# Performance work log

Measured on AMD Instinct MI355X. Metric: run time of the kernel, lower is better.

The kernel has to match this reference:

```python
import jax, jax.numpy as jnp
import numpy as np

# distilled LLaVA-style decoder: nf4-quantized linears + LoRA(q/k/v/o) + gumbel-softmax -> embedding einsum
B, S, D, H, L = 1, 2048, 2048, 16, 2
DH = D // H
DFF, V, R, BLK = 8192, 32000, 8, 64
LORA_SCALE = 16.0 / R  # alpha / r
TAU = 1.0
SQRT_DH = float(np.sqrt(DH))

# bitsandbytes NF4 codebook (16 values)
NF4 = jnp.array([-1.0, -0.6961928009986877, -0.5250730514526367, -0.39491748809814453,
                 -0.28444138169288635, -0.18477343022823334, -0.09105003625154495, 0.0,
                 0.07958029955625534, 0.16093020141124725, 0.24611230194568634,
                 0.33791524171829224, 0.44070982933044434, 0.5626170039176941,
                 0.7229568362236023, 1.0], dtype=jnp.float32)


def dequant(idx, scale):
    # idx [..., out, in] int in [0,16); scale [..., out, in//BLK] per-block absmax
    return NF4[idx] * jnp.repeat(scale, BLK, axis=-1)


def rmsnorm(x, w):
    return x * jax.lax.rsqrt(jnp.mean(x * x, axis=-1, keepdims=True) + 1e-6) * w


def setup_inputs():
    key = jax.random.key(0)
    k = jax.random.split(key, 12)
    return {
        "input_ids": jax.random.randint(k[0], (B, S), 0, V, dtype=jnp.int32),
        "u": jax.random.uniform(k[1], (B, S, V), dtype=jnp.float32),
        "emb": jax.random.normal(k[2], (V, D), dtype=jnp.float32) * 0.02,
        "attn_scale": jax.random.uniform(k[3], (L, 4, D, D // BLK), minval=0.005, maxval=0.02, dtype=jnp.float32),
        "ffn_gu_scale": jax.random.uniform(k[4], (L, 2, DFF, D // BLK), minval=0.005, maxval=0.02, dtype=jnp.float32),
        "ffn_d_scale": jax.random.uniform(k[5], (L, D, DFF // BLK), minval=0.005, maxval=0.02, dtype=jnp.float32),
        "lora_A": jax.random.normal(k[6], (L, 4, R, D), dtype=jnp.float32) * 0.01,
        "lora_B": jax.random.normal(k[7], (L, 4, D, R), dtype=jnp.float32) * 0.01,
        "norm_w": jnp.ones((L, 2, D), dtype=jnp.float32),
        "final_norm_w": jnp.ones((D,), dtype=jnp.float32),
        "attn_idx": jax.random.randint(k[8], (L, 4, D, D), 0, 16, dtype=jnp.int32),
        "ffn_gu_idx": jax.random.randint(k[9], (L, 2, DFF, D), 0, 16, dtype=jnp.int32),
        "ffn_d_idx": jax.random.randint(k[10], (L, D, DFF), 0, 16, dtype=jnp.int32),
    }


def reference(input_ids, u, emb, attn_scale, ffn_gu_scale, ffn_d_scale,
              lora_A, lora_B, norm_w, final_norm_w, attn_idx, ffn_gu_idx, ffn_d_idx):
    h = emb[input_ids]  # [B, S, D]
    causal = jnp.tril(jnp.ones((S, S), dtype=bool))
    for l in range(L):
        x = rmsnorm(h, norm_w[l, 0])
        w = dequant(attn_idx[l], attn_scale[l])  # [4, D, D] dequantized q/k/v/o weights

        def proj(i, t):
            # nf4 linear + LoRA adapter (y = t W^T + (t A^T) B^T * alpha/r)
            return t @ w[i].T + ((t @ lora_A[l, i].T) @ lora_B[l, i].T) * LORA_SCALE

        q = proj(0, x).reshape(B, S, H, DH)
        k_ = proj(1, x).reshape(B, S, H, DH)
        v = proj(2, x).reshape(B, S, H, DH)
        scores = jnp.einsum('bqhd,bkhd->bhqk', q, k_) / SQRT_DH
        scores = jnp.where(causal, scores, -1e30)
        p = jax.nn.softmax(scores, axis=-1)
        o = jnp.einsum('bhqk,bkhd->bqhd', p, v).reshape(B, S, D)
        h = h + proj(3, o)

        x = rmsnorm(h, norm_w[l, 1])
        wgu = dequant(ffn_gu_idx[l], ffn_gu_scale[l])  # [2, DFF, D] gate/up
        wd = dequant(ffn_d_idx[l], ffn_d_scale[l])     # [D, DFF] down
        h = h + (jax.nn.silu(x @ wgu[0].T) * (x @ wgu[1].T)) @ wd.T

    h = rmsnorm(h, final_norm_w)
    logits = h @ emb.T  # [B, S, V]
    # gumbel_softmax(tau, hard=False): softmax((logits + G)/tau), G = -log(-log(U))
    gnoise = -jnp.log(-jnp.log(u + 1e-10) + 1e-10)
    g = jax.nn.softmax((logits + gnoise) / TAU, axis=-1)
    soft_embeddings = jnp.einsum('bsv,vd->bsd', g, emb)
    return soft_embeddings, logits
```

## Files before the change

### kernel.cpp

```cpp
#include <hip/hip_runtime.h>
#include <hip/hip_bf16.h>

typedef unsigned short u16;
typedef unsigned int u32;
typedef __bf16 bf16t;
typedef bf16t bf16x8 __attribute__((ext_vector_type(8)));
typedef float f32x4 __attribute__((ext_vector_type(4)));

constexpr int S_   = 2048;
constexpr int D_   = 2048;
constexpr int H_   = 16;
constexpr int DH_  = 128;
constexpr int L_   = 2;
constexpr int DFF_ = 8192;
constexpr int V_   = 32000;
constexpr int R_   = 8;

#define MFMA16(a, b, c) __builtin_amdgcn_mfma_f32_16x16x32_bf16(a, b, c, 0, 0, 0)

__constant__ float c_nf4[16] = {
  -1.0f, -0.6961928009986877f, -0.5250730514526367f, -0.39491748809814453f,
  -0.28444138169288635f, -0.18477343022823334f, -0.09105003625154495f, 0.0f,
  0.07958029955625534f, 0.16093020141124725f, 0.24611230194568634f,
  0.33791524171829224f, 0.44070982933044434f, 0.5626170039176941f,
  0.7229568362236023f, 1.0f };

__device__ __forceinline__ u16 f2bf(float f) {
  union { float f; u32 u; } v; v.f = f;
  u32 r = v.u + 0x7fffu + ((v.u >> 16) & 1u);
  return (u16)(r >> 16);
}
__device__ __forceinline__ float bf2f(u16 h) {
  union { u32 u; float f; } v; v.u = ((u32)h) << 16; return v.f;
}

__global__ __launch_bounds__(256) void k_gather(const int* __restrict__ ids,
                                                const float* __restrict__ emb,
                                                float* __restrict__ h) {
  int t = blockIdx.x * 256 + threadIdx.x;
  int s = t >> 11;
  int d = t & 2047;
  h[t] = emb[(size_t)ids[s] * D_ + d];
}

__global__ __launch_bounds__(256) void k_rmsnorm(const float* __restrict__ in,
                                                 const float* __restrict__ w,
                                                 u16* __restrict__ out) {
  int s = blockIdx.x;
  const float* x = in + (size_t)s * D_;
  float ss = 0.f;
  for (int d = threadIdx.x; d < D_; d += 256) { float v = x[d]; ss += v * v; }
#pragma unroll
  for (int m = 1; m < 64; m <<= 1) ss += __shfl_xor(ss, m, 64);
  __shared__ float sh[4];
  if ((threadIdx.x & 63) == 0) sh[threadIdx.x >> 6] = ss;
  __syncthreads();
  ss = sh[0] + sh[1] + sh[2] + sh[3];
  float sc = rsqrtf(ss * (1.0f / D_) + 1e-6f);
  u16* o = out + (size_t)s * D_;
  for (int d = threadIdx.x; d < D_; d += 256) o[d] = f2bf(x[d] * sc * w[d]);
}

__global__ __launch_bounds__(256) void k_dequant(const int* __restrict__ idx,
                                                 const float* __restrict__ scale,
                                                 u16* __restrict__ out, int kshift) {
  size_t t = (size_t)blockIdx.x * 256 + threadIdx.x;
  size_t e = t * 8;
  int k = (int)(e & ((1u << kshift) - 1));
  size_t n = e >> kshift;
  float s = scale[(n << (kshift - 6)) + (k >> 6)];
  int4 i0 = *(const int4*)(idx + e);
  int4 i1 = *(const int4*)(idx + e + 4);
  uint4 o;
  o.x = (u32)f2bf(c_nf4[i0.x] * s) | ((u32)f2bf(c_nf4[i0.y] * s) << 16);
  o.y = (u32)f2bf(c_nf4[i0.z] * s) | ((u32)f2bf(c_nf4[i0.w] * s) << 16);
  o.z = (u32)f2bf(c_nf4[i1.x] * s) | ((u32)f2bf(c_nf4[i1.y] * s) << 16);
  o.w = (u32)f2bf(c_nf4[i1.z] * s) | ((u32)f2bf(c_nf4[i1.w] * s) << 16);
  *(uint4*)(out + e) = o;
}

__global__ __launch_bounds__(256) void k_f2b(const float* __restrict__ src,
                                             u16* __restrict__ dst) {
  size_t e = ((size_t)blockIdx.x * 256 + threadIdx.x) * 8;
  float4 f0 = *(const float4*)(src + e);
  float4 f1 = *(const float4*)(src + e + 4);
  uint4 o;
  o.x = (u32)f2bf(f0.x) | ((u32)f2bf(f0.y) << 16);
  o.y = (u32)f2bf(f0.z) | ((u32)f2bf(f0.w) << 16);
  o.z = (u32)f2bf(f1.x) | ((u32)f2bf(f1.y) << 16);
  o.w = (u32)f2bf(f1.z) | ((u32)f2bf(f1.w) << 16);
  *(uint4*)(dst + e) = o;
}

__global__ __launch_bounds__(256) void k_transpose(const float* __restrict__ src,
                                                   u16* __restrict__ dst) {
  __shared__ u16 tile[64][65];
  int v0 = blockIdx.x * 64, d0 = blockIdx.y * 64;
  int tid = threadIdx.x;
  int rr = tid >> 4, cc = (tid & 15) * 4;
#pragma unroll
  for (int j = 0; j < 4; ++j) {
    int r = j * 16 + rr;
    float4 f = *(const float4*)(src + (size_t)(v0 + r) * D_ + d0 + cc);
    tile[r][cc + 0] = f2bf(f.x); tile[r][cc + 1] = f2bf(f.y);
    tile[r][cc + 2] = f2bf(f.z); tile[r][cc + 3] = f2bf(f.w);
  }
  __syncthreads();
#pragma unroll
  for (int j = 0; j < 4; ++j) {
    int r = j * 16 + rr;
    ushort4 w;
    w.x = tile[cc + 0][r]; w.y = tile[cc + 1][r];
    w.z = tile[cc + 2][r]; w.w = tile[cc + 3][r];
    *(ushort4*)(dst + (size_t)(d0 + r) * V_ + v0 + cc) = w;
  }
}

enum { OUT_F32 = 0, OUT_F32_ACC = 1, OUT_BF16 = 2 };

template<int OUTMODE>
__global__ __launch_bounds__(512, 2) void k_gemm256(const u16* __restrict__ A, int lda,
                                                    const u16* __restrict__ B, int ldb,
                                                    void* __restrict__ Cv, int ldc,
                                                    int Kc, size_t zstride) {
  __shared__ u16 As[2][256][64];
  __shared__ u16 Bs[2][256][64];
  const int tid = threadIdx.x;
  const int lane = tid & 63, w = tid >> 6;
  const int wr = w >> 2, wc = w & 3;
  const int g = (lane >> 4), l15 = lane & 15, sl7 = lane & 7;

  const int gx = gridDim.x, gy = gridDim.y;
  const int cpx = (gx * gy) >> 3;
  int d = blockIdx.y * gx + blockIdx.x;
  int swz = (d & 7) * cpx + (d >> 3);
  const int m0 = (swz % gy) * 256;
  const int n0 = (swz / gy) * 256;

  A += (size_t)blockIdx.z * Kc;
  B += (size_t)blockIdx.z * Kc;
  float* Cf = (float*)Cv + (size_t)blockIdx.z * zstride;

  const int NT = Kc >> 6;
  const int srow = w * 8 + (lane >> 3);
  const int sch  = (lane & 7) ^ (lane >> 3);

  auto stageA = [&](int half, int tile) {
    const u16* src = A + (size_t)(m0 + half * 128 + srow) * lda + tile * 64 + sch * 8;
    u16* dst = &As[tile & 1][half * 128 + w * 8][0];
#pragma unroll
    for (int rnd = 0; rnd < 2; ++rnd)
      __builtin_amdgcn_global_load_lds(
          (const __attribute__((address_space(1))) void*)(src + (size_t)rnd * 64 * lda),
          (__attribute__((address_space(3))) void*)(dst + rnd * 64 * 64), 16, 0, 0);
  };
  auto stageB = [&](int half, int tile) {
    const u16* src = B + (size_t)(n0 + half * 128 + srow) * ldb + tile * 64 + sch * 8;
    u16* dst = &Bs[tile & 1][half * 128 + w * 8][0];
#pragma unroll
    for (int rnd = 0; rnd < 2; ++rnd)
      __builtin_amdgcn_global_load_lds(
          (const __attribute__((address_space(1))) void*)(src + (size_t)rnd * 64 * ldb),
          (__attribute__((address_space(3))) void*)(dst + rnd * 64 * 64), 16, 0, 0);
  };

  f32x4 acc[8][4] = {};
  bf16x8 areg[4][2], breg[2][2][2];

  stageB(0, 0); stageB(1, 0); stageA(0, 0); stageA(1, 0);
  if (NT > 1) {
    stageB(0, 1); stageB(1, 1); stageA(0, 1); stageA(1, 1);
    asm volatile("s_waitcnt vmcnt(8)" ::: "memory");
  } else {
    asm volatile("s_waitcnt vmcnt(0)" ::: "memory");
  }
  __builtin_amdgcn_s_barrier();

#define LOADA(QR)                                                                   \
  _Pragma("unroll") for (int m = 0; m < 4; ++m)                                     \
    _Pragma("unroll") for (int kh = 0; kh < 2; ++kh) {                              \
      int hr = wr * 128 + (QR) * 64 + m * 16 + l15;                                 \
      areg[m][kh] = *(const bf16x8*)(abase + hr * 64 + ((((kh << 2) | g) ^ sl7) << 3)); \
    }
#define LOADB(QC)                                                                   \
  _Pragma("unroll") for (int n = 0; n < 2; ++n)                                     \
    _Pragma("unroll") for (int kh = 0; kh < 2; ++kh) {                              \
      int br = wc * 64 + (QC) * 32 + n * 16 + l15;                                  \
      breg[QC][n][kh] = *(const bf16x8*)(bbase + br * 64 + ((((kh << 2) | g) ^ sl7) << 3)); \
    }
#define QPHASE(QR, QC)                                                              \
  __builtin_amdgcn_s_setprio(1);                                                    \
  _Pragma("unroll") for (int m = 0; m < 4; ++m)                                     \
    _Pragma("unroll") for (int n = 0; n < 2; ++n)                                   \
      _Pragma("unroll") for (int kh = 0; kh < 2; ++kh)                              \
        acc[(QR) * 4 + m][(QC) * 2 + n] = __builtin_amdgcn_mfma_f32_16x16x32_bf16(  \
            areg[m][kh], breg[QC][n][kh], acc[(QR) * 4 + m][(QC) * 2 + n], 0, 0, 0); \
  __builtin_amdgcn_s_setprio(0);

  for (int t = 0; t < NT; ++t) {
    const u16* abase = &As[t & 1][0][0];
    const u16* bbase = &Bs[t & 1][0][0];
    LOADA(0); LOADB(0);
    __builtin_amdgcn_s_barrier();
    asm volatile("s_waitcnt lgkmcnt(0)" ::: "memory");
    QPHASE(0, 0);
    __builtin_amdgcn_s_barrier();
    LOADB(1);
    __builtin_amdgcn_s_barrier();
    asm volatile("s_waitcnt lgkmcnt(0)" ::: "memory");
    QPHASE(0, 1);
    __builtin_amdgcn_s_barrier();
    LOADA(1);
    if (t + 2 < NT) { stageB(0, t + 2); stageB(1, t + 2); }
    __builtin_amdgcn_s_barrier();
    asm volatile("s_waitcnt lgkmcnt(0)" ::: "memory");
    QPHASE(1, 1);
    __builtin_amdgcn_s_barrier();
    if (t + 2 < NT) { stageA(0, t + 2); stageA(1, t + 2); }
    QPHASE(1, 0);
    if (t + 1 < NT) {
      if (t + 2 < NT) asm volatile("s_waitcnt vmcnt(8)" ::: "memory");
      else            asm volatile("s_waitcnt vmcnt(0)" ::: "memory");
    }
    __builtin_amdgcn_s_barrier();
  }
#undef LOADA
#undef LOADB
#undef QPHASE

  const int er = g * 4;
#pragma unroll
  for (int i = 0; i < 8; ++i)
#pragma unroll
    for (int j = 0; j < 4; ++j)
#pragma unroll
      for (int r = 0; r < 4; ++r) {
        int row = m0 + wr * 128 + i * 16 + er + r;
        int col = n0 + wc * 64 + j * 16 + l15;
        if (OUTMODE == OUT_BF16) {
          ((u16*)Cv)[(size_t)row * ldc + col] = f2bf(acc[i][j][r]);
        } else if (OUTMODE == OUT_F32_ACC) {
          Cf[(size_t)row * ldc + col] += acc[i][j][r];
        } else {
          Cf[(size_t)row * ldc + col] = acc[i][j][r];
        }
      }
}

__global__ __launch_bounds__(256) void k_red(const float* __restrict__ P,
                                             float* __restrict__ dst, int accmode) {
  size_t i = ((size_t)blockIdx.x * 256 + threadIdx.x) * 4;
  const size_t n = (size_t)4 * 1024 * 1024;
  float4 a = *(const float4*)(P + i);
  float4 b = *(const float4*)(P + n + i);
  float4 c = *(const float4*)(P + 2 * n + i);
  float4 d = *(const float4*)(P + 3 * n + i);
  float4 r;
  r.x = (a.x + b.x) + (c.x + d.x);
  r.y = (a.y + b.y) + (c.y + d.y);
  r.z = (a.z + b.z) + (c.z + d.z);
  r.w = (a.w + b.w) + (c.w + d.w);
  if (accmode) {
    float4 o = *(const float4*)(dst + i);
    r.x += o.x; r.y += o.y; r.z += o.z; r.w += o.w;
  }
  *(float4*)(dst + i) = r;
}

__global__ __launch_bounds__(256) void k_lora_down(const u16* __restrict__ X,
                                                   const float* __restrict__ A,
                                                   float* __restrict__ T, int nproj) {
  int s = blockIdx.x;
  int lane = threadIdx.x & 63, wv = threadIdx.x >> 6;
  const u16* x = X + (size_t)s * D_;
  for (int p = wv; p < nproj * R_; p += 4) {
    const float* a = A + (size_t)p * D_;
    float sum = 0.f;
    for (int d = lane; d < D_; d += 64) sum += bf2f(x[d]) * a[d];
#pragma unroll
    for (int m = 1; m < 64; m <<= 1) sum += __shfl_xor(sum, m, 64);
    if (lane == 0) T[(size_t)s * (nproj * R_) + p] = sum;
  }
}

__global__ __launch_bounds__(256) void k_lora_up(float* __restrict__ Y, int ystride,
                                                 const float* __restrict__ T,
                                                 const float* __restrict__ Bm, int nproj) {
  int t = blockIdx.x * 256 + threadIdx.x;
  int d = t & (D_ - 1);
  int si = t >> 11;
  int i = si % nproj;
  int s = si / nproj;
  const float* tp = T + ((size_t)s * nproj + i) * R_;
  const float* bp = Bm + ((size_t)i * D_ + d) * R_;
  float acc = 0.f;
#pragma unroll
  for (int r = 0; r < R_; r++) acc += tp[r] * bp[r];
  Y[(size_t)s * ystride + (size_t)i * D_ + d] += 2.0f * acc;
}

__global__ __launch_bounds__(256) void k_lora_up_qkv(u16* __restrict__ qkvb,
                                                     const float* __restrict__ T,
                                                     const float* __restrict__ Bm) {
  size_t t = ((size_t)blockIdx.x * 256 + threadIdx.x) * 8;
  int c = (int)(t % 6144);
  int s = (int)(t / 6144);
  int i = c >> 11, dd = c & 2047;
  const float* tp = T + ((size_t)s * 3 + i) * R_;
  float tr[8];
#pragma unroll
  for (int r = 0; r < R_; ++r) tr[r] = tp[r];
  uint4 q = *(const uint4*)(qkvb + t);
  u16 qs[8] = {(u16)(q.x & 0xffff), (u16)(q.x >> 16), (u16)(q.y & 0xffff), (u16)(q.y >> 16),
               (u16)(q.z & 0xffff), (u16)(q.z >> 16), (u16)(q.w & 0xffff), (u16)(q.w >> 16)};
  u16 os[8];
#pragma unroll
  for (int j = 0; j < 8; ++j) {
    const float* bp = Bm + ((size_t)i * D_ + dd + j) * R_;
    float a = 0.f;
#pragma unroll
    for (int r = 0; r < R_; ++r) a += tr[r] * bp[r];
    os[j] = f2bf(bf2f(qs[j]) + 2.0f * a);
  }
  uint4 o;
  o.x = (u32)os[0] | ((u32)os[1] << 16);
  o.y = (u32)os[2] | ((u32)os[3] << 16);
  o.z = (u32)os[4] | ((u32)os[5] << 16);
  o.w = (u32)os[6] | ((u32)os[7] << 16);
  *(uint4*)(qkvb + t) = o;
}

__global__ __launch_bounds__(256) void k_vtrans(const u16* __restrict__ qkvb,
                                                u16* __restrict__ Vt) {
  __shared__ u16 t[64][136];
  int s0 = blockIdx.x * 64, hh = blockIdx.y;
  int tid = threadIdx.x;
#pragma unroll
  for (int it = 0; it < 4; ++it) {
    int e = it * 2048 + tid * 8;
    int sr = e >> 7, sc = e & 127;
    *(uint4*)&t[sr][sc] =
        *(const uint4*)(qkvb + (size_t)(s0 + sr) * 6144 + 4096 + hh * 128 + sc);
  }
  __syncthreads();
#pragma unroll
  for (int it = 0; it < 4; ++it) {
    int q = it * 256 + tid;
    int dh = q >> 3, sc = (q & 7) * 8;
    u16 e0 = t[sc + 0][dh], e1 = t[sc + 1][dh], e2 = t[sc + 2][dh], e3 = t[sc + 3][dh];
    u16 e4 = t[sc + 4][dh], e5 = t[sc + 5][dh], e6 = t[sc + 6][dh], e7 = t[sc + 7][dh];
    uint4 o;
    o.x = (u32)e0 | ((u32)e1 << 16);
    o.y = (u32)e2 | ((u32)e3 << 16);
    o.z = (u32)e4 | ((u32)e5 << 16);
    o.w = (u32)e6 | ((u32)e7 << 16);
    *(uint4*)(Vt + ((size_t)hh * DH_ + dh) * S_ + s0 + sc) = o;
  }
}

__global__ __launch_bounds__(256) void k_attn2(const u16* __restrict__ qkvb,
                                               const u16* __restrict__ Vt,
                                               u16* __restrict__ out) {
  __shared__ u16 Ks[2][64 * 128];
  __shared__ u16 VTs[2][128 * 64];
  __shared__ u16 PT[4][64 * 16];
  const int tid = threadIdx.x;
  const int lane = tid & 63, w = tid >> 6;
  const int g = lane >> 4, l4 = lane & 15;
  const int p = blockIdx.x;
  const int hh = blockIdx.y;
  const int ld = 6144;
  const float rs = 0.08838834764831845f;
  const int qa0 = p * 64, qb0 = (31 - p) * 64;
  const int ntb = 32 - p;
  char* pt_w = (char*)&PT[w][0];

  const int qga = qa0 + w * 16 + l4;
  const int qgb = qb0 + w * 16 + l4;

  bf16x8 qfa[4], qfb[4];
#pragma unroll
  for (int kh = 0; kh < 4; ++kh) {
    qfa[kh] = *(const bf16x8*)(qkvb + (size_t)qga * ld + hh * DH_ + kh * 32 + g * 8);
    qfb[kh] = *(const bf16x8*)(qkvb + (size_t)qgb * ld + hh * DH_ + kh * 32 + g * 8);
  }

  float ma = -3.0e38f, la = 0.f, mb = -3.0e38f, lb = 0.f;
  f32x4 acc_a[8] = {}, acc_b[8] = {};
  bf16x8 pba[2], pbb[2];

  auto stage = [&](int buf, int kt) {
    const int kv0 = kt * 64;
#pragma unroll
    for (int i = 0; i < 4; ++i) {
      int rl = (w * 4 + i) * 4 + (lane >> 4);
      int cs = (lane & 15) ^ ((rl & 7) ^ (((rl >> 3) & 3) << 1));
      __builtin_amdgcn_global_load_lds(
          (const __attribute__((address_space(1))) void*)(
              qkvb + (size_t)(kv0 + rl) * ld + 2048 + hh * DH_ + cs * 8),
          (__attribute__((address_space(3))) void*)(&Ks[buf][(w * 4 + i) * 512]), 16, 0, 0);
    }
#pragma unroll
    for (int i = 0; i < 4; ++i) {
      int dh = (w * 4 + i) * 8 + (lane >> 3);
      int cs = (lane & 7) ^ (dh & 7);
      __builtin_amdgcn_global_load_lds(
          (const __attribute__((address_space(1))) void*)(
              Vt + ((size_t)hh * DH_ + dh) * S_ + kv0 + cs * 8),
          (__attribute__((address_space(3))) void*)(&VTs[buf][(w * 4 + i) * 512]), 16, 0, 0);
    }
  };

  auto softpb = [&](f32x4* sv, float& m, float& l, f32x4* acc, int qg, bool diag,
                    int kv0, bf16x8* pb) {
    float pv[16];
    float tmax = -3.0e38f;
#pragma unroll
    for (int kb = 0; kb < 4; ++kb)
#pragma unroll
      for (int r = 0; r < 4; ++r) {
        float s = sv[kb][r] * rs;
        if (diag) {
          int kglob = kv0 + kb * 16 + g * 4 + r;
          if (kglob > qg) s = -1.0e30f;
        }
        pv[kb * 4 + r] = s;
        tmax = fmaxf(tmax, s);
      }
    tmax = fmaxf(tmax, __shfl_xor(tmax, 16, 64));
    tmax = fmaxf(tmax, __shfl_xor(tmax, 32, 64));
    float mn = fmaxf(m, tmax);
    float corr = __expf(m - mn);
    m = mn;
    float ps = 0.f;
#pragma unroll
    for (int i = 0; i < 16; ++i) { pv[i] = __expf(pv[i] - mn); ps += pv[i]; }
    ps += __shfl_xor(ps, 16, 64);
    ps += __shfl_xor(ps, 32, 64);
    l = l * corr + ps;
#pragma unroll
    for (int f = 0; f < 8; ++f) {
      acc[f][0] *= corr; acc[f][1] *= corr; acc[f][2] *= corr; acc[f][3] *= corr;
    }
#pragma unroll
    for (int kb = 0; kb < 4; ++kb)
#pragma unroll
      for (int r = 0; r < 4; ++r) {
        int key = kb * 16 + g * 4 + r;
        int byte = (key * 32 + l4 * 2) ^ (((key >> 3) & 3) << 5);
        *(u16*)(pt_w + byte) = f2bf(pv[kb * 4 + r]);
      }
#pragma unroll
    for (int ks = 0; ks < 2; ++ks) {
      union { bf16x8 v; u16 s[8]; } ub;
#pragma unroll
      for (int j = 0; j < 8; ++j) {
        int key = ks * 32 + g * 8 + j;
        int byte = (key * 32 + l4 * 2) ^ (((key >> 3) & 3) << 5);
        ub.s[j] = *(const u16*)(pt_w + byte);
      }
      pb[ks] = ub.v;
    }
  };

  stage(0, 0);
  asm volatile("s_waitcnt vmcnt(0)" ::: "memory");
  __syncthreads();

  for (int kt = 0; kt < ntb; ++kt) {
    const int kv0 = kt * 64;
    const int buf = kt & 1;
    if (kt + 1 < ntb) stage(buf ^ 1, kt + 1);

    const char* kb_base = (const char*)&Ks[buf][0];
    const char* vb_base = (const char*)&VTs[buf][0];
    const bool doa = (kt <= p);

    f32x4 sa[4] = {}, sb[4] = {};
#pragma unroll
    for (int kb = 0; kb < 4; ++kb) {
#pragma unroll
      for (int kh = 0; kh < 4; ++kh) {
        int key = kb * 16 + l4;
        int ch = (kh * 4 + g) ^ ((key & 7) ^ (((key >> 3) & 3) << 1));
        bf16x8 af = *(const bf16x8*)(kb_base + key * 256 + ch * 16);
        if (doa) sa[kb] = MFMA16(af, qfa[kh], sa[kb]);
        sb[kb] = MFMA16(af, qfb[kh], sb[kb]);
      }
    }

    if (doa) softpb(sa, ma, la, acc_a, qga, kt == p, kv0, pba);
    softpb(sb, mb, lb, acc_b, qgb, kt == ntb - 1, kv0, pbb);

#pragma unroll
    for (int f = 0; f < 8; ++f) {
#pragma unroll
      for (int ks = 0; ks < 2; ++ks) {
        int dh = f * 16 + l4;
        int ch = (ks * 4 + g) ^ (dh & 7);
        bf16x8 va = *(const bf16x8*)(vb_base + dh * 128 + ch * 16);
        if (doa) acc_a[f] = MFMA16(va, pba[ks], acc_a[f]);
        acc_b[f] = MFMA16(va, pbb[ks], acc_b[f]);
      }
    }

    if (kt + 1 < ntb) {
      asm volatile("s_waitcnt vmcnt(0)" ::: "memory");
      __syncthreads();
    }
  }

  float inva = 1.f / la, invb = 1.f / lb;
  u16* opa = out + (size_t)qga * D_ + hh * DH_;
  u16* opb = out + (size_t)qgb * D_ + hh * DH_;
#pragma unroll
  for (int f = 0; f < 8; ++f)
#pragma unroll
    for (int r = 0; r < 4; ++r) {
      opa[f * 16 + g * 4 + r] = f2bf(acc_a[f][r] * inva);
      opb[f * 16 + g * 4 + r] = f2bf(acc_b[f][r] * invb);
    }
}

__global__ __launch_bounds__(256) void k_silumul(u16* __restrict__ gu) {
  size_t i = ((size_t)blockIdx.x * 256 + threadIdx.x) * 4;
  int s = (int)(i >> 13);
  int f = (int)(i & 8191);
  u16* gp = gu + (size_t)s * (2 * DFF_) + f;
  ushort4 gt = *(ushort4*)gp;
  ushort4 up = *(ushort4*)(gp + DFF_);
  float g0 = bf2f(gt.x), g1 = bf2f(gt.y), g2 = bf2f(gt.z), g3 = bf2f(gt.w);
  float u0 = bf2f(up.x), u1 = bf2f(up.y), u2 = bf2f(up.z), u3 = bf2f(up.w);
  ushort4 o;
  o.x = f2bf(g0 / (1.f + __expf(-g0)) * u0);
  o.y = f2bf(g1 / (1.f + __expf(-g1)) * u1);
  o.z = f2bf(g2 / (1.f + __expf(-g2)) * u2);
  o.w = f2bf(g3 / (1.f + __expf(-g3)) * u3);
  *(ushort4*)gp = o;
}

__global__ __launch_bounds__(256) void k_gumbel(const float* __restrict__ logits,
                                                const float* __restrict__ u,
                                                u16* __restrict__ g) {
  __shared__ float z[V_];
  __shared__ float sred[4];
  int s = blockIdx.x;
  const float* lp = logits + (size_t)s * V_;
  const float* up = u + (size_t)s * V_;
  float m = -3.0e38f;
  for (int v4 = threadIdx.x; v4 < V_ / 4; v4 += 256) {
    float4 lv = *(const float4*)(lp + v4 * 4);
    float4 uv = *(const float4*)(up + v4 * 4);
    float z0 = lv.x - __logf(-__logf(uv.x + 1e-10f) + 1e-10f);
    float z1 = lv.y - __logf(-__logf(uv.y + 1e-10f) + 1e-10f);
    float z2 = lv.z - __logf(-__logf(uv.z + 1e-10f) + 1e-10f);
    float z3 = lv.w - __logf(-__logf(uv.w + 1e-10f) + 1e-10f);
    *(float4*)(z + v4 * 4) = make_float4(z0, z1, z2, z3);
    m = fmaxf(fmaxf(fmaxf(m, z0), fmaxf(z1, z2)), z3);
  }
#pragma unroll
  for (int msk = 1; msk < 64; msk <<= 1) m = fmaxf(m, __shfl_xor(m, msk, 64));
  if ((threadIdx.x & 63) == 0) sred[threadIdx.x >> 6] = m;
  __syncthreads();
  float M = fmaxf(fmaxf(sred[0], sred[1]), fmaxf(sred[2], sred[3]));
  float l = 0.f;
  for (int v4 = threadIdx.x; v4 < V_ / 4; v4 += 256) {
    float4 zv = *(float4*)(z + v4 * 4);
    zv.x = __expf(zv.x - M); zv.y = __expf(zv.y - M);
    zv.z = __expf(zv.z - M); zv.w = __expf(zv.w - M);
    *(float4*)(z + v4 * 4) = zv;
    l += (zv.x + zv.y) + (zv.z + zv.w);
  }
#pragma unroll
  for (int msk = 1; msk < 64; msk <<= 1) l += __shfl_xor(l, msk, 64);
  __syncthreads();
  if ((threadIdx.x & 63) == 0) sred[threadIdx.x >> 6] = l;
  __syncthreads();
  float inv = 1.f / (sred[0] + sred[1] + sred[2] + sred[3]);
  u16* gp = g + (size_t)s * V_;
  for (int v4 = threadIdx.x; v4 < V_ / 4; v4 += 256) {
    float4 zv = *(float4*)(z + v4 * 4);
    ushort4 o;
    o.x = f2bf(zv.x * inv); o.y = f2bf(zv.y * inv);
    o.z = f2bf(zv.z * inv); o.w = f2bf(zv.w * inv);
    *(ushort4*)(gp + v4 * 4) = o;
  }
}

extern "C" void kernel_launch(void* const* d_in, const int* in_sizes, int n_in,
                              void* d_out, int out_size, void* d_ws, size_t ws_size,
                              hipStream_t stream) {
  const int*   ids        = (const int*)d_in[0];
  const float* u          = (const float*)d_in[1];
  const float* emb        = (const float*)d_in[2];
  const float* attn_scale = (const float*)d_in[3];
  const float* gu_scale   = (const float*)d_in[4];
  const float* dn_scale   = (const float*)d_in[5];
  const float* lora_A     = (const float*)d_in[6];
  const float* lora_B     = (const float*)d_in[7];
  const float* norm_w     = (const float*)d_in[8];
  const float* fnorm_w    = (const float*)d_in[9];
  const int*   attn_idx   = (const int*)d_in[10];
  const int*   gu_idx     = (const int*)d_in[11];
  const int*   dn_idx     = (const int*)d_in[12];

  float* out_se = (float*)d_out;
  float* out_lg = (float*)d_out + (size_t)S_ * D_;

  char* W = (char*)d_ws;
  float* h    = (float*)(W);
  u16*   xb   = (u16*)(W + ((size_t)16 << 20));
  u16*   qkvb = (u16*)(W + ((size_t)72 << 20));
  u16*   Vtb  = (u16*)(W + ((size_t)96 << 20));
  u16*   ob   = (u16*)(W + ((size_t)104 << 20));
  u16*   gub  = (u16*)(W + ((size_t)112 << 20));
  u16*   wdq  = (u16*)(W + ((size_t)176 << 20));
  float* Tl   = (float*)(W + ((size_t)240 << 20));
  u16*   embb = (u16*)(W);
  u16*   gsm  = (u16*)(W + ((size_t)125 << 20));
  u16*   embT = (u16*)(W);
  u16*   xbh  = (u16*)d_out;
  float* Pk   = (float*)(W + ((size_t)250 << 20));
  const bool big = ws_size >= ((size_t)314 << 20);
  const size_t ZS = (size_t)4 * 1024 * 1024;

  dim3 b256(256), b512(512);

  k_gather<<<dim3(S_ * D_ / 256), b256, 0, stream>>>(ids, emb, h);

  for (int l = 0; l < L_; ++l) {
    const int*   aidx = attn_idx + (size_t)l * 4 * D_ * D_;
    const float* ascl = attn_scale + (size_t)l * 4 * D_ * (D_ / 64);
    const float* lA   = lora_A + (size_t)l * 4 * R_ * D_;
    const float* lB   = lora_B + (size_t)l * 4 * D_ * R_;

    k_rmsnorm<<<dim3(S_), b256, 0, stream>>>(h, norm_w + (size_t)l * 2 * D_, xb);
    k_dequant<<<dim3(4 * D_ * D_ / 8 / 256), b256, 0, stream>>>(aidx, ascl, wdq, 11);
    k_gemm256<OUT_BF16><<<dim3(3 * D_ / 256, 8), b512, 0, stream>>>(
        xb, D_, wdq, D_, qkvb, 3 * D_, D_, 0);
    k_lora_down<<<dim3(S_), b256, 0, stream>>>(xb, lA, Tl, 3);
    k_lora_up_qkv<<<dim3(S_ * 3 * D_ / 8 / 256), b256, 0, stream>>>(qkvb, Tl, lB);
    k_vtrans<<<dim3(S_ / 64, H_), b256, 0, stream>>>(qkvb, Vtb);
    k_attn2<<<dim3(16, H_), b256, 0, stream>>>(qkvb, Vtb, ob);
    k_gemm256<OUT_F32_ACC><<<dim3(D_ / 256, 8), b512, 0, stream>>>(
        ob, D_, wdq + (size_t)3 * D_ * D_, D_, h, D_, D_, 0);
    k_lora_down<<<dim3(S_), b256, 0, stream>>>(ob, lA + (size_t)3 * R_ * D_, Tl, 1);
    k_lora_up<<<dim3(S_ * D_ / 256), b256, 0, stream>>>(h, D_, Tl, lB + (size_t)3 * D_ * R_, 1);

    k_rmsnorm<<<dim3(S_), b256, 0, stream>>>(h, norm_w + (size_t)l * 2 * D_ + D_, xb);
    k_dequant<<<dim3(2 * DFF_ * D_ / 8 / 256), b256, 0, stream>>>(
        gu_idx + (size_t)l * 2 * DFF_ * D_, gu_scale + (size_t)l * 2 * DFF_ * (D_ / 64), wdq, 11);
    k_gemm256<OUT_BF16><<<dim3(2 * DFF_ / 256, 8), b512, 0, stream>>>(
        xb, D_, wdq, D_, gub, 2 * DFF_, D_, 0);
    k_silumul<<<dim3(S_ * DFF_ / 4 / 256), b256, 0, stream>>>(gub);
    k_dequant<<<dim3(D_ * DFF_ / 8 / 256), b256, 0, stream>>>(
        dn_idx + (size_t)l * D_ * DFF_, dn_scale + (size_t)l * D_ * (DFF_ / 64), wdq, 13);
    if (big) {
      k_gemm256<OUT_F32><<<dim3(D_ / 256, 8, 4), b512, 0, stream>>>(
          gub, 2 * DFF_, wdq, DFF_, Pk, D_, DFF_ / 4, ZS);
      k_red<<<dim3(4096), b256, 0, stream>>>(Pk, h, 1);
    } else {
      k_gemm256<OUT_F32_ACC><<<dim3(D_ / 256, 8), b512, 0, stream>>>(
          gub, 2 * DFF_, wdq, DFF_, h, D_, DFF_, 0);
    }
  }

  k_rmsnorm<<<dim3(S_), b256, 0, stream>>>(h, fnorm_w, xbh);
  k_f2b<<<dim3(V_ * D_ / 8 / 256), b256, 0, stream>>>(emb, embb);
  k_gemm256<OUT_F32><<<dim3(V_ / 256, 8), b512, 0, stream>>>(
      xbh, D_, embb, D_, out_lg, V_, D_, 0);
  k_gumbel<<<dim3(S_), b256, 0, stream>>>(out_lg, u, gsm);
  k_transpose<<<dim3(V_ / 64, D_ / 64), b256, 0, stream>>>(emb, embT);
  if (big) {
    k_gemm256<OUT_F32><<<dim3(D_ / 256, 8, 4), b512, 0, stream>>>(
        gsm, V_, embT, V_, Pk, D_, V_ / 4, ZS);
    k_red<<<dim3(4096), b256, 0, stream>>>(Pk, out_se, 0);
  } else {
    k_gemm256<OUT_F32><<<dim3(D_ / 256, 8), b512, 0, stream>>>(
        gsm, V_, embT, V_, out_se, D_, V_, 0);
  }
}
```

Measured before the change: 2.443 ms.

## Fuse embedding prep, split-K o-proj, and spread GEMM staging across phases

Merges the fp32->bf16 embedding conversion and the transpose into one kernel that writes both layouts from a single read of emb. To make room, the gsm and embT workspace buffers swap places. The GEMM now issues its global->LDS staging loads across all four compute phases instead of two, with vmcnt thresholds adjusted to match, and it changes the warp-to-subtile mapping so each quadrant is spread across warps. The attention output projection uses split-K with a reduction when the workspace is large, giving 64 blocks more parallelism at the cost of an extra reduction pass and partial-sum traffic.

```diff
diff --git a/kernel.cpp b/kernel.cpp
--- a/kernel.cpp
+++ b/kernel.cpp
@@ -79,21 +79,9 @@
   *(uint4*)(out + e) = o;
 }
 
-__global__ __launch_bounds__(256) void k_f2b(const float* __restrict__ src,
-                                             u16* __restrict__ dst) {
-  size_t e = ((size_t)blockIdx.x * 256 + threadIdx.x) * 8;
-  float4 f0 = *(const float4*)(src + e);
-  float4 f1 = *(const float4*)(src + e + 4);
-  uint4 o;
-  o.x = (u32)f2bf(f0.x) | ((u32)f2bf(f0.y) << 16);
-  o.y = (u32)f2bf(f0.z) | ((u32)f2bf(f0.w) << 16);
-  o.z = (u32)f2bf(f1.x) | ((u32)f2bf(f1.y) << 16);
-  o.w = (u32)f2bf(f1.z) | ((u32)f2bf(f1.w) << 16);
-  *(uint4*)(dst + e) = o;
-}
-
-__global__ __launch_bounds__(256) void k_transpose(const float* __restrict__ src,
-                                                   u16* __restrict__ dst) {
+__global__ __launch_bounds__(256) void k_embprep(const float* __restrict__ src,
+                                                 u16* __restrict__ embb,
+                                                 u16* __restrict__ embT) {
   __shared__ u16 tile[64][65];
   int v0 = blockIdx.x * 64, d0 = blockIdx.y * 64;
   int tid = threadIdx.x;
@@ -102,8 +90,11 @@
   for (int j = 0; j < 4; ++j) {
     int r = j * 16 + rr;
     float4 f = *(const float4*)(src + (size_t)(v0 + r) * D_ + d0 + cc);
-    tile[r][cc + 0] = f2bf(f.x); tile[r][cc + 1] = f2bf(f.y);
-    tile[r][cc + 2] = f2bf(f.z); tile[r][cc + 3] = f2bf(f.w);
+    u16 b0 = f2bf(f.x), b1 = f2bf(f.y), b2 = f2bf(f.z), b3 = f2bf(f.w);
+    tile[r][cc + 0] = b0; tile[r][cc + 1] = b1;
+    tile[r][cc + 2] = b2; tile[r][cc + 3] = b3;
+    ushort4 wv; wv.x = b0; wv.y = b1; wv.z = b2; wv.w = b3;
+    *(ushort4*)(embb + (size_t)(v0 + r) * D_ + d0 + cc) = wv;
   }
   __syncthreads();
 #pragma unroll
@@ -112,7 +103,7 @@
     ushort4 w;
     w.x = tile[cc + 0][r]; w.y = tile[cc + 1][r];
     w.z = tile[cc + 2][r]; w.w = tile[cc + 3][r];
-    *(ushort4*)(dst + (size_t)(d0 + r) * V_ + v0 + cc) = w;
+    *(ushort4*)(embT + (size_t)(d0 + r) * V_ + v0 + cc) = w;
   }
 }
 
@@ -167,10 +158,10 @@
   f32x4 acc[8][4] = {};
   bf16x8 areg[4][2], breg[2][2][2];
 
-  stageB(0, 0); stageB(1, 0); stageA(0, 0); stageA(1, 0);
+  stageB(0, 0); stageA(0, 0); stageB(1, 0); stageA(1, 0);
   if (NT > 1) {
-    stageB(0, 1); stageB(1, 1); stageA(0, 1); stageA(1, 1);
-    asm volatile("s_waitcnt vmcnt(8)" ::: "memory");
+    stageB(0, 1); stageA(0, 1); stageB(1, 1);
+    asm volatile("s_waitcnt vmcnt(6)" ::: "memory");
   } else {
     asm volatile("s_waitcnt vmcnt(0)" ::: "memory");
   }
@@ -179,13 +170,13 @@
 #define LOADA(QR)                                                                   \
   _Pragma("unroll") for (int m = 0; m < 4; ++m)                                     \
     _Pragma("unroll") for (int kh = 0; kh < 2; ++kh) {                              \
-      int hr = wr * 128 + (QR) * 64 + m * 16 + l15;                                 \
+      int hr = (QR) * 128 + wr * 64 + m * 16 + l15;                                 \
       areg[m][kh] = *(const bf16x8*)(abase + hr * 64 + ((((kh << 2) | g) ^ sl7) << 3)); \
     }
 #define LOADB(QC)                                                                   \
   _Pragma("unroll") for (int n = 0; n < 2; ++n)                                     \
     _Pragma("unroll") for (int kh = 0; kh < 2; ++kh) {                              \
-      int br = wc * 64 + (QC) * 32 + n * 16 + l15;                                  \
+      int br = (QC) * 128 + wc * 32 + n * 16 + l15;                                 \
       breg[QC][n][kh] = *(const bf16x8*)(bbase + br * 64 + ((((kh << 2) | g) ^ sl7) << 3)); \
     }
 #define QPHASE(QR, QC)                                                              \
@@ -201,25 +192,27 @@
     const u16* abase = &As[t & 1][0][0];
     const u16* bbase = &Bs[t & 1][0][0];
     LOADA(0); LOADB(0);
+    if (t + 1 < NT) stageA(1, t + 1);
     __builtin_amdgcn_s_barrier();
     asm volatile("s_waitcnt lgkmcnt(0)" ::: "memory");
     QPHASE(0, 0);
     __builtin_amdgcn_s_barrier();
     LOADB(1);
+    if (t + 2 < NT) stageB(0, t + 2);
     __builtin_amdgcn_s_barrier();
     asm volatile("s_waitcnt lgkmcnt(0)" ::: "memory");
     QPHASE(0, 1);
     __builtin_amdgcn_s_barrier();
     LOADA(1);
-    if (t + 2 < NT) { stageB(0, t + 2); stageB(1, t + 2); }
+    if (t + 2 < NT) stageA(0, t + 2);
     __builtin_amdgcn_s_barrier();
     asm volatile("s_waitcnt lgkmcnt(0)" ::: "memory");
     QPHASE(1, 1);
     __builtin_amdgcn_s_barrier();
-    if (t + 2 < NT) { stageA(0, t + 2); stageA(1, t + 2); }
+    if (t + 2 < NT) stageB(1, t + 2);
     QPHASE(1, 0);
     if (t + 1 < NT) {
-      if (t + 2 < NT) asm volatile("s_waitcnt vmcnt(8)" ::: "memory");
+      if (t + 2 < NT) asm volatile("s_waitcnt vmcnt(6)" ::: "memory");
       else            asm volatile("s_waitcnt vmcnt(0)" ::: "memory");
     }
     __builtin_amdgcn_s_barrier();
@@ -235,8 +228,8 @@
     for (int j = 0; j < 4; ++j)
 #pragma unroll
       for (int r = 0; r < 4; ++r) {
-        int row = m0 + wr * 128 + i * 16 + er + r;
-        int col = n0 + wc * 64 + j * 16 + l15;
+        int row = m0 + (i >> 2) * 128 + wr * 64 + (i & 3) * 16 + er + r;
+        int col = n0 + (j >> 1) * 128 + wc * 32 + (j & 1) * 16 + l15;
         if (OUTMODE == OUT_BF16) {
           ((u16*)Cv)[(size_t)row * ldc + col] = f2bf(acc[i][j][r]);
         } else if (OUTMODE == OUT_F32_ACC) {
@@ -617,8 +610,8 @@
   u16*   wdq  = (u16*)(W + ((size_t)176 << 20));
   float* Tl   = (float*)(W + ((size_t)240 << 20));
   u16*   embb = (u16*)(W);
-  u16*   gsm  = (u16*)(W + ((size_t)125 << 20));
-  u16*   embT = (u16*)(W);
+  u16*   gsm  = (u16*)(W);
+  u16*   embT = (u16*)(W + ((size_t)125 << 20));
   u16*   xbh  = (u16*)d_out;
   float* Pk   = (float*)(W + ((size_t)250 << 20));
   const bool big = ws_size >= ((size_t)314 << 20);
@@ -642,8 +635,14 @@
     k_lora_up_qkv<<<dim3(S_ * 3 * D_ / 8 / 256), b256, 0, stream>>>(qkvb, Tl, lB);
     k_vtrans<<<dim3(S_ / 64, H_), b256, 0, stream>>>(qkvb, Vtb);
     k_attn2<<<dim3(16, H_), b256, 0, stream>>>(qkvb, Vtb, ob);
-    k_gemm256<OUT_F32_ACC><<<dim3(D_ / 256, 8), b512, 0, stream>>>(
-        ob, D_, wdq + (size_t)3 * D_ * D_, D_, h, D_, D_, 0);
+    if (big) {
+      k_gemm256<OUT_F32><<<dim3(D_ / 256, 8, 4), b512, 0, stream>>>(
+          ob, D_, wdq + (size_t)3 * D_ * D_, D_, Pk, D_, D_ / 4, ZS);
+      k_red<<<dim3(4096), b256, 0, stream>>>(Pk, h, 1);
+    } else {
+      k_gemm256<OUT_F32_ACC><<<dim3(D_ / 256, 8), b512, 0, stream>>>(
+          ob, D_, wdq + (size_t)3 * D_ * D_, D_, h, D_, D_, 0);
+    }
     k_lora_down<<<dim3(S_), b256, 0, stream>>>(ob, lA + (size_t)3 * R_ * D_, Tl, 1);
     k_lora_up<<<dim3(S_ * D_ / 256), b256, 0, stream>>>(h, D_, Tl, lB + (size_t)3 * D_ * R_, 1);
 
@@ -666,11 +665,10 @@
   }
 
   k_rmsnorm<<<dim3(S_), b256, 0, stream>>>(h, fnorm_w, xbh);
-  k_f2b<<<dim3(V_ * D_ / 8 / 256), b256, 0, stream>>>(emb, embb);
+  k_embprep<<<dim3(V_ / 64, D_ / 64), b256, 0, stream>>>(emb, embb, embT);
   k_gemm256<OUT_F32><<<dim3(V_ / 256, 8), b512, 0, stream>>>(
       xbh, D_, embb, D_, out_lg, V_, D_, 0);
   k_gumbel<<<dim3(S_), b256, 0, stream>>>(out_lg, u, gsm);
-  k_transpose<<<dim3(V_ / 64, D_ / 64), b256, 0, stream>>>(emb, embT);
   if (big) {
     k_gemm256<OUT_F32><<<dim3(D_ / 256, 8, 4), b512, 0, stream>>>(
         gsm, V_, embT, V_, Pk, D_, V_ / 4, ZS);
```

New measurement: 2.390 ms. -2.2%, faster.
